# Optimization experiments

Measured on AMD Instinct MI355X. Metric: run time of the kernel, lower is better.

Reference implementation:

```python
import jax, jax.numpy as jnp
import numpy as np

HIDDEN = 1024
HEADS = 16
HEAD = HIDDEN // HEADS


def setup_inputs() -> dict:
    key = jax.random.key(0)
    ks = jax.random.split(key, 6)
    B, T = 2, 2048
    x = jax.random.normal(ks[0], (B, T, HIDDEN), dtype=jnp.float32)
    mask = jnp.ones((T, T), dtype=jnp.float32)
    s = 1.0 / np.sqrt(HIDDEN)
    Wqkv = jax.random.normal(ks[1], (HIDDEN, 3 * HIDDEN), dtype=jnp.float32) * s
    bqkv = jnp.zeros((3 * HIDDEN,), dtype=jnp.float32)
    Wproj = jax.random.normal(ks[2], (HIDDEN, HIDDEN), dtype=jnp.float32) * s
    bproj = jnp.zeros((HIDDEN,), dtype=jnp.float32)
    return {"x": x, "mask": mask, "Wqkv": Wqkv, "bqkv": bqkv,
            "Wproj": Wproj, "bproj": bproj}


def reference(x, mask, Wqkv, bqkv, Wproj, bproj):
    B, T, C = x.shape
    qkv = x @ Wqkv + bqkv                      # [B,T,3C]
    q, k, v = jnp.split(qkv, 3, axis=-1)
    def heads(t):                              # [B,T,C] -> [B,H,T,D]
        return t.reshape(B, T, HEADS, HEAD).transpose(0, 2, 1, 3)
    q, k, v = heads(q), heads(k), heads(v)
    scores = jnp.einsum('bhqd,bhkd->bhqk', q, k) / np.sqrt(HEAD)
    scores = jnp.where(mask == 0, -jnp.inf, scores)
    attn = jax.nn.softmax(scores, axis=-1)
    out = jnp.einsum('bhqk,bhkd->bhqd', attn, v)
    out = out.transpose(0, 2, 1, 3).reshape(B, T, C)
    return out @ Wproj + bproj
```

## Files before the change

kernel.cpp:

```cpp
#include <hip/hip_runtime.h>
#include <stdint.h>

#define HID 1024
#define NH 16
#define HD 64
#define BATCH 2
#define SEQ 2048
#define MR (BATCH*SEQ)
#define NQKV (3*HID)

typedef __attribute__((ext_vector_type(8))) _Float16 h16x8;
typedef __attribute__((ext_vector_type(2))) __fp16 fp16x2;
typedef __attribute__((ext_vector_type(8))) unsigned short u16x8;
typedef __attribute__((ext_vector_type(4))) float f32x4;

#if __has_builtin(__builtin_amdgcn_exp2f)
#define EXP2(x) __builtin_amdgcn_exp2f(x)
#else
#define EXP2(x) exp2f(x)
#endif

static __device__ __forceinline__ unsigned short f2h(float f) {
  union { _Float16 h; unsigned short u; } v; v.h = (_Float16)f; return v.u;
}
static __device__ __forceinline__ unsigned pk2(float a, float b) {
  union { fp16x2 h; unsigned u; } v;
  v.h = __builtin_amdgcn_cvt_pkrtz(a, b);
  return v.u;
}

typedef const __attribute__((address_space(1))) unsigned int glb_u32;
typedef __attribute__((address_space(3))) unsigned int lds_u32;
static __device__ __forceinline__ void cp16(const void* g, void* l) {
  __builtin_amdgcn_global_load_lds((glb_u32*)g, (lds_u32*)l, 16, 0, 0);
}

#define QSCL (0.125f * 1.44269504f)

__global__ __launch_bounds__(256) void k_cvt(const float4* __restrict__ src,
                                             ushort4* __restrict__ dst) {
  int i = blockIdx.x * 256 + threadIdx.x;
  float4 v = src[i];
  ushort4 h;
  h.x = f2h(v.x); h.y = f2h(v.y); h.z = f2h(v.z); h.w = f2h(v.w);
  dst[i] = h;
}

__global__ __launch_bounds__(256) void k_transpose_h(const float* __restrict__ src,
                                                     int R, int C,
                                                     unsigned short* __restrict__ dst) {
  __shared__ float tile[32][33];
  int tx = threadIdx.x, ty = threadIdx.y;
  int col0 = blockIdx.x * 32, row0 = blockIdx.y * 32;
  #pragma unroll
  for (int i = 0; i < 32; i += 8)
    tile[ty + i][tx] = src[(size_t)(row0 + ty + i) * C + col0 + tx];
  __syncthreads();
  #pragma unroll
  for (int i = 0; i < 32; i += 8) {
    float v = tile[tx][ty + i];
    dst[(size_t)(col0 + ty + i) * R + row0 + tx] = f2h(v);
  }
}

__global__ __launch_bounds__(256) void k_maskbits(const float* __restrict__ mask,
                                                  unsigned long long* __restrict__ mb) {
  int gw = blockIdx.x * 4 + (threadIdx.x >> 6);
  int lane = threadIdx.x & 63;
  float v = mask[(size_t)gw * 64 + lane];
  unsigned long long b = __ballot(v != 0.f);
  if (lane == 0) mb[gw] = b;
}

__global__ __launch_bounds__(256) void k_gemm_qkv(const unsigned short* __restrict__ A,
                                                  const unsigned short* __restrict__ Bt,
                                                  const float* __restrict__ bias,
                                                  unsigned short* __restrict__ Qp,
                                                  unsigned short* __restrict__ Kp,
                                                  unsigned short* __restrict__ Vt) {
  const int K = HID;
  int tid = threadIdx.x;
  int wave = tid >> 6, lane = tid & 63, quad = lane >> 4, l16 = lane & 15;
  int wm = wave >> 1, wn = wave & 1;
  int m0 = blockIdx.y * 128, n0 = blockIdx.x * 128;
  __shared__ __align__(16) unsigned short As[128 * 32], Bs[128 * 32];
  f32x4 acc[4][4] = {};
  for (int k0 = 0; k0 < K; k0 += 32) {
    __syncthreads();
    #pragma unroll
    for (int i = 0; i < 2; i++) {
      int c = tid + i * 256;
      int r = c >> 2, co = (c & 3) << 3;
      cp16(&A[(size_t)(m0 + r) * K + k0 + co], &As[c << 3]);
      cp16(&Bt[(size_t)(n0 + r) * K + k0 + co], &Bs[c << 3]);
    }
    __syncthreads();
    h16x8 af[4], bf[4];
    #pragma unroll
    for (int i = 0; i < 4; i++) {
      af[i] = *(const h16x8*)&As[(wm * 64 + i * 16 + l16) * 32 + quad * 8];
      bf[i] = *(const h16x8*)&Bs[(wn * 64 + i * 16 + l16) * 32 + quad * 8];
    }
    #pragma unroll
    for (int i = 0; i < 4; i++)
      #pragma unroll
      for (int j = 0; j < 4; j++)
        acc[i][j] = __builtin_amdgcn_mfma_f32_16x16x32_f16(af[i], bf[j], acc[i][j], 0, 0, 0);
  }
  #pragma unroll
  for (int j = 0; j < 4; j++) {
    int n = n0 + wn * 64 + j * 16 + l16;
    float bv = bias[n];
    int which = n >> 10;
    int rem = n & 1023;
    int h = rem >> 6, d = rem & 63;
    if (which == 2) {
      #pragma unroll
      for (int i = 0; i < 4; i++) {
        int m = m0 + wm * 64 + i * 16 + quad * 4;
        int b = m >> 11, t = m & 2047;
        uint2 tt;
        tt.x = pk2(acc[i][j][0] + bv, acc[i][j][1] + bv);
        tt.y = pk2(acc[i][j][2] + bv, acc[i][j][3] + bv);
        *(uint2*)&Vt[(size_t)(b * NH + h) * (SEQ * HD) + (size_t)d * SEQ + t] = tt;
      }
    } else {
      #pragma unroll
      for (int i = 0; i < 4; i++)
        #pragma unroll
        for (int r = 0; r < 4; r++) {
          int m = m0 + wm * 64 + i * 16 + quad * 4 + r;
          int b = m >> 11, t = m & 2047;
          float val = acc[i][j][r] + bv;
          int hb = b * NH + h;
          if (which == 0) Qp[(size_t)hb * (SEQ * HD) + (size_t)t * HD + d] = f2h(val * QSCL);
          else            Kp[(size_t)hb * (SEQ * HD) + (size_t)t * HD + d] = f2h(val);
        }
    }
  }
}

__global__ __launch_bounds__(256) void k_attn(const unsigned short* __restrict__ Qp,
                                              const unsigned short* __restrict__ Kp,
                                              const unsigned short* __restrict__ Vt,
                                              const unsigned long long* __restrict__ mb,
                                              unsigned short* __restrict__ AO) {
  int tid = threadIdx.x, wave = tid >> 6, lane = tid & 63, quad = lane >> 4, l16 = lane & 15;
  int bh = blockIdx.y, qbase = blockIdx.x * 64;
  const unsigned short* Qg = Qp + (size_t)bh * (SEQ * HD);
  const unsigned short* Kg = Kp + (size_t)bh * (SEQ * HD);
  const unsigned short* Vg = Vt + (size_t)bh * (SEQ * HD);
  __shared__ __align__(16) unsigned short smem[16896];
  unsigned short* Qs = smem;
  unsigned short* Ks = smem + 4096;
  unsigned short* Vs = smem + 8192;
  unsigned short* Ps = smem + 12288 + wave * (16 * 72);
  unsigned short* Os = smem + 4096;

  #pragma unroll
  for (int i = 0; i < 2; i++) {
    int c = tid + i * 256;
    int row = c >> 3, sc = ((c ^ row) & 7) << 3;
    cp16(&Qg[(size_t)(qbase + row) * HD + sc], &Qs[c << 3]);
  }
  int qrow = qbase + wave * 16 + l16;
  const unsigned long long* mrow = mb + (size_t)qrow * 32;
  float m_i = -3.0e38f, l_i = 0.f;
  f32x4 acc_o[4] = {};
  int x7 = l16 & 7;

  for (int kt = 0; kt < 32; kt++) {
    int kbase = kt * 64;
    __syncthreads();
    #pragma unroll
    for (int i = 0; i < 2; i++) {
      int c = tid + i * 256;
      int row = c >> 3, sc = ((c ^ row) & 7) << 3;
      cp16(&Kg[(size_t)(kbase + row) * HD + sc], &Ks[c << 3]);
      cp16(&Vg[(size_t)row * SEQ + kbase + sc], &Vs[c << 3]);
    }
    unsigned long long w = mrow[kt];
    __syncthreads();
    f32x4 s[4] = {};
    h16x8 bq[2];
    #pragma unroll
    for (int kk = 0; kk < 2; kk++)
      bq[kk] = *(const h16x8*)&Qs[(wave * 16 + l16) * 64 + (((kk * 4 + quad) ^ x7) << 3)];
    #pragma unroll
    for (int nt = 0; nt < 4; nt++)
      #pragma unroll
      for (int kk = 0; kk < 2; kk++) {
        h16x8 a = *(const h16x8*)&Ks[(nt * 16 + l16) * 64 + (((kk * 4 + quad) ^ x7) << 3)];
        s[nt] = __builtin_amdgcn_mfma_f32_16x16x32_f16(a, bq[kk], s[nt], 0, 0, 0);
      }
    if (!__all(w == ~0ULL)) {
      #pragma unroll
      for (int nt = 0; nt < 4; nt++)
        #pragma unroll
        for (int r = 0; r < 4; r++)
          if (!((w >> (nt * 16 + quad * 4 + r)) & 1ULL)) s[nt][r] = -1e30f;
    }
    float v = s[0][0];
    #pragma unroll
    for (int nt = 0; nt < 4; nt++)
      #pragma unroll
      for (int r = 0; r < 4; r++) v = fmaxf(v, s[nt][r]);
    v = fmaxf(v, __shfl_xor(v, 16));
    v = fmaxf(v, __shfl_xor(v, 32));
    float mnew = fmaxf(m_i, v);
    float alpha = EXP2(m_i - mnew);
    m_i = mnew;
    float lsum = 0.f;
    #pragma unroll
    for (int nt = 0; nt < 4; nt++)
      #pragma unroll
      for (int r = 0; r < 4; r++) {
        s[nt][r] = EXP2(s[nt][r] - mnew);
        lsum += s[nt][r];
      }
    lsum += __shfl_xor(lsum, 16);
    lsum += __shfl_xor(lsum, 32);
    l_i = l_i * alpha + lsum;
    #pragma unroll
    for (int nt = 0; nt < 4; nt++)
      #pragma unroll
      for (int r = 0; r < 4; r++) acc_o[nt][r] *= alpha;
    #pragma unroll
    for (int nt = 0; nt < 4; nt++) {
      uint2 t;
      t.x = pk2(s[nt][0], s[nt][1]);
      t.y = pk2(s[nt][2], s[nt][3]);
      *(uint2*)&Ps[l16 * 72 + nt * 16 + quad * 4] = t;
    }
    h16x8 bp[2];
    #pragma unroll
    for (int kk = 0; kk < 2; kk++)
      bp[kk] = *(const h16x8*)&Ps[l16 * 72 + kk * 32 + quad * 8];
    #pragma unroll
    for (int nt = 0; nt < 4; nt++)
      #pragma unroll
      for (int kk = 0; kk < 2; kk++) {
        h16x8 a = *(const h16x8*)&Vs[(nt * 16 + l16) * 64 + (((kk * 4 + quad) ^ x7) << 3)];
        acc_o[nt] = __builtin_amdgcn_mfma_f32_16x16x32_f16(a, bp[kk], acc_o[nt], 0, 0, 0);
      }
  }
  float rl = 1.0f / l_i;
  __syncthreads();
  #pragma unroll
  for (int nt = 0; nt < 4; nt++) {
    uint2 t;
    t.x = (unsigned)f2h(acc_o[nt][0] * rl) | ((unsigned)f2h(acc_o[nt][1] * rl) << 16);
    t.y = (unsigned)f2h(acc_o[nt][2] * rl) | ((unsigned)f2h(acc_o[nt][3] * rl) << 16);
    *(uint2*)&Os[(wave * 16 + l16) * 72 + nt * 16 + quad * 4] = t;
  }
  __syncthreads();
  int b = bh >> 4, h = bh & 15;
  #pragma unroll
  for (int i = 0; i < 2; i++) {
    int c = tid + i * 256;
    int row = c >> 3, co = (c & 7) << 3;
    u16x8 vv = *(const u16x8*)&Os[row * 72 + co];
    *(u16x8*)&AO[(size_t)(b * SEQ + qbase + row) * HID + h * HD + co] = vv;
  }
}

__global__ __launch_bounds__(256) void k_gemm_proj(const unsigned short* __restrict__ A,
                                                   const unsigned short* __restrict__ Bt,
                                                   const float* __restrict__ bias,
                                                   float* __restrict__ out) {
  const int K = HID;
  int tid = threadIdx.x;
  int wave = tid >> 6, lane = tid & 63, quad = lane >> 4, l16 = lane & 15;
  int wm = wave >> 1, wn = wave & 1;
  int m0 = blockIdx.y * 128, n0 = blockIdx.x * 128;
  __shared__ __align__(16) unsigned short As[128 * 32], Bs[128 * 32];
  f32x4 acc[4][4] = {};
  for (int k0 = 0; k0 < K; k0 += 32) {
    __syncthreads();
    #pragma unroll
    for (int i = 0; i < 2; i++) {
      int c = tid + i * 256;
      int r = c >> 2, co = (c & 3) << 3;
      cp16(&A[(size_t)(m0 + r) * K + k0 + co], &As[c << 3]);
      cp16(&Bt[(size_t)(n0 + r) * K + k0 + co], &Bs[c << 3]);
    }
    __syncthreads();
    h16x8 af[4], bf[4];
    #pragma unroll
    for (int i = 0; i < 4; i++) {
      af[i] = *(const h16x8*)&As[(wm * 64 + i * 16 + l16) * 32 + quad * 8];
      bf[i] = *(const h16x8*)&Bs[(wn * 64 + i * 16 + l16) * 32 + quad * 8];
    }
    #pragma unroll
    for (int i = 0; i < 4; i++)
      #pragma unroll
      for (int j = 0; j < 4; j++)
        acc[i][j] = __builtin_amdgcn_mfma_f32_16x16x32_f16(af[i], bf[j], acc[i][j], 0, 0, 0);
  }
  #pragma unroll
  for (int j = 0; j < 4; j++) {
    int n = n0 + wn * 64 + j * 16 + l16;
    float bv = bias[n];
    #pragma unroll
    for (int i = 0; i < 4; i++)
      #pragma unroll
      for (int r = 0; r < 4; r++) {
        int m = m0 + wm * 64 + i * 16 + quad * 4 + r;
        out[(size_t)m * HID + n] = acc[i][j][r] + bv;
      }
  }
}

extern "C" void kernel_launch(void* const* d_in, const int* in_sizes, int n_in,
                              void* d_out, int out_size, void* d_ws, size_t ws_size,
                              hipStream_t stream) {
  const float* x     = (const float*)d_in[0];
  const float* mask  = (const float*)d_in[1];
  const float* Wqkv  = (const float*)d_in[2];
  const float* bqkv  = (const float*)d_in[3];
  const float* Wproj = (const float*)d_in[4];
  const float* bproj = (const float*)d_in[5];
  float* out = (float*)d_out;

  uint8_t* ws = (uint8_t*)d_ws;
  size_t off = 0;
  auto alloc = [&](size_t bytes) -> void* {
    void* p = (void*)(ws + off);
    off += (bytes + 255) & ~(size_t)255;
    return p;
  };
  unsigned short* xh   = (unsigned short*)alloc((size_t)MR * HID * 2);
  unsigned short* WqT  = (unsigned short*)alloc((size_t)NQKV * HID * 2);
  unsigned short* WpT  = (unsigned short*)alloc((size_t)HID * HID * 2);
  unsigned short* Qp   = (unsigned short*)alloc((size_t)BATCH * NH * SEQ * HD * 2);
  unsigned short* Kp   = (unsigned short*)alloc((size_t)BATCH * NH * SEQ * HD * 2);
  unsigned short* Vtp  = (unsigned short*)alloc((size_t)BATCH * NH * SEQ * HD * 2);
  unsigned short* AO   = (unsigned short*)alloc((size_t)MR * HID * 2);
  unsigned long long* mb = (unsigned long long*)alloc((size_t)SEQ * (SEQ / 64) * 8);

  k_cvt<<<MR * HID / 4 / 256, 256, 0, stream>>>((const float4*)x, (ushort4*)xh);
  k_transpose_h<<<dim3(NQKV / 32, HID / 32), dim3(32, 8), 0, stream>>>(Wqkv, HID, NQKV, WqT);
  k_transpose_h<<<dim3(HID / 32, HID / 32), dim3(32, 8), 0, stream>>>(Wproj, HID, HID, WpT);
  k_maskbits<<<SEQ * (SEQ / 64) / 4, 256, 0, stream>>>(mask, mb);
  k_gemm_qkv<<<dim3(NQKV / 128, MR / 128), 256, 0, stream>>>(xh, WqT, bqkv, Qp, Kp, Vtp);
  k_attn<<<dim3(SEQ / 64, BATCH * NH), 256, 0, stream>>>(Qp, Kp, Vtp, mb, AO);
  k_gemm_proj<<<dim3(HID / 128, MR / 128), 256, 0, stream>>>(AO, WpT, bproj, out);
}
```

Baseline: 234.6 us.

## Double K-tile depth in GEMMs with XOR swizzle and process 128 keys per attention step

Both GEMM kernels now stage 64-wide K tiles instead of 32, with an XOR-swizzled shared-memory layout. This halves the number of barrier pairs per tile and is meant to reduce LDS bank conflicts on the fragment reads. The attention kernel loads two 64-key K/V tiles per iteration, which halves the barriers and online-softmax rescales, and it hoists the Q fragment loads out of the loop. In exchange it uses more shared memory, which may lower occupancy, and more registers for the doubled score fragments.

```diff
diff --git a/kernel.cpp b/kernel.cpp
--- a/kernel.cpp
+++ b/kernel.cpp
@@ -82,30 +82,34 @@
   int tid = threadIdx.x;
   int wave = tid >> 6, lane = tid & 63, quad = lane >> 4, l16 = lane & 15;
   int wm = wave >> 1, wn = wave & 1;
+  int x7 = l16 & 7;
   int m0 = blockIdx.y * 128, n0 = blockIdx.x * 128;
-  __shared__ __align__(16) unsigned short As[128 * 32], Bs[128 * 32];
+  __shared__ __align__(16) unsigned short As[128 * 64], Bs[128 * 64];
   f32x4 acc[4][4] = {};
-  for (int k0 = 0; k0 < K; k0 += 32) {
-    __syncthreads();
-    #pragma unroll
-    for (int i = 0; i < 2; i++) {
+  for (int k0 = 0; k0 < K; k0 += 64) {
+    __syncthreads();
+    #pragma unroll
+    for (int i = 0; i < 4; i++) {
       int c = tid + i * 256;
-      int r = c >> 2, co = (c & 3) << 3;
-      cp16(&A[(size_t)(m0 + r) * K + k0 + co], &As[c << 3]);
-      cp16(&Bt[(size_t)(n0 + r) * K + k0 + co], &Bs[c << 3]);
-    }
-    __syncthreads();
-    h16x8 af[4], bf[4];
-    #pragma unroll
-    for (int i = 0; i < 4; i++) {
-      af[i] = *(const h16x8*)&As[(wm * 64 + i * 16 + l16) * 32 + quad * 8];
-      bf[i] = *(const h16x8*)&Bs[(wn * 64 + i * 16 + l16) * 32 + quad * 8];
-    }
-    #pragma unroll
-    for (int i = 0; i < 4; i++)
-      #pragma unroll
-      for (int j = 0; j < 4; j++)
-        acc[i][j] = __builtin_amdgcn_mfma_f32_16x16x32_f16(af[i], bf[j], acc[i][j], 0, 0, 0);
+      int r = c >> 3, sc = ((c ^ r) & 7) << 3;
+      cp16(&A[(size_t)(m0 + r) * K + k0 + sc], &As[c << 3]);
+      cp16(&Bt[(size_t)(n0 + r) * K + k0 + sc], &Bs[c << 3]);
+    }
+    __syncthreads();
+    #pragma unroll
+    for (int kc = 0; kc < 2; kc++) {
+      h16x8 af[4], bf[4];
+      #pragma unroll
+      for (int i = 0; i < 4; i++) {
+        af[i] = *(const h16x8*)&As[(wm * 64 + i * 16 + l16) * 64 + (((kc * 4 + quad) ^ x7) << 3)];
+        bf[i] = *(const h16x8*)&Bs[(wn * 64 + i * 16 + l16) * 64 + (((kc * 4 + quad) ^ x7) << 3)];
+      }
+      #pragma unroll
+      for (int i = 0; i < 4; i++)
+        #pragma unroll
+        for (int j = 0; j < 4; j++)
+          acc[i][j] = __builtin_amdgcn_mfma_f32_16x16x32_f16(af[i], bf[j], acc[i][j], 0, 0, 0);
+    }
   }
   #pragma unroll
   for (int j = 0; j < 4; j++) {
@@ -150,12 +154,14 @@
   const unsigned short* Qg = Qp + (size_t)bh * (SEQ * HD);
   const unsigned short* Kg = Kp + (size_t)bh * (SEQ * HD);
   const unsigned short* Vg = Vt + (size_t)bh * (SEQ * HD);
-  __shared__ __align__(16) unsigned short smem[16896];
-  unsigned short* Qs = smem;
-  unsigned short* Ks = smem + 4096;
-  unsigned short* Vs = smem + 8192;
-  unsigned short* Ps = smem + 12288 + wave * (16 * 72);
-  unsigned short* Os = smem + 4096;
+  __shared__ __align__(16) unsigned short smem[25088];
+  unsigned short* Qs  = smem;
+  unsigned short* Ks0 = smem + 4096;
+  unsigned short* Ks1 = smem + 8192;
+  unsigned short* Vs0 = smem + 12288;
+  unsigned short* Vs1 = smem + 16384;
+  unsigned short* Ps  = smem + 20480 + wave * (16 * 72);
+  unsigned short* Os  = smem + 4096;
 
   #pragma unroll
   for (int i = 0; i < 2; i++) {
@@ -169,42 +175,50 @@
   f32x4 acc_o[4] = {};
   int x7 = l16 & 7;
 
-  for (int kt = 0; kt < 32; kt++) {
-    int kbase = kt * 64;
+  __syncthreads();
+  h16x8 bq[2];
+  #pragma unroll
+  for (int kk = 0; kk < 2; kk++)
+    bq[kk] = *(const h16x8*)&Qs[(wave * 16 + l16) * 64 + (((kk * 4 + quad) ^ x7) << 3)];
+
+  for (int kt = 0; kt < 16; kt++) {
+    int kbase = kt * 128;
     __syncthreads();
     #pragma unroll
     for (int i = 0; i < 2; i++) {
       int c = tid + i * 256;
       int row = c >> 3, sc = ((c ^ row) & 7) << 3;
-      cp16(&Kg[(size_t)(kbase + row) * HD + sc], &Ks[c << 3]);
-      cp16(&Vg[(size_t)row * SEQ + kbase + sc], &Vs[c << 3]);
-    }
-    unsigned long long w = mrow[kt];
-    __syncthreads();
-    f32x4 s[4] = {};
-    h16x8 bq[2];
-    #pragma unroll
-    for (int kk = 0; kk < 2; kk++)
-      bq[kk] = *(const h16x8*)&Qs[(wave * 16 + l16) * 64 + (((kk * 4 + quad) ^ x7) << 3)];
+      cp16(&Kg[(size_t)(kbase + row) * HD + sc],      &Ks0[c << 3]);
+      cp16(&Kg[(size_t)(kbase + 64 + row) * HD + sc], &Ks1[c << 3]);
+      cp16(&Vg[(size_t)row * SEQ + kbase + sc],       &Vs0[c << 3]);
+      cp16(&Vg[(size_t)row * SEQ + kbase + 64 + sc],  &Vs1[c << 3]);
+    }
+    unsigned long long w0 = mrow[2 * kt], w1 = mrow[2 * kt + 1];
+    __syncthreads();
+    f32x4 s0[4] = {}, s1[4] = {};
     #pragma unroll
     for (int nt = 0; nt < 4; nt++)
       #pragma unroll
       for (int kk = 0; kk < 2; kk++) {
-        h16x8 a = *(const h16x8*)&Ks[(nt * 16 + l16) * 64 + (((kk * 4 + quad) ^ x7) << 3)];
-        s[nt] = __builtin_amdgcn_mfma_f32_16x16x32_f16(a, bq[kk], s[nt], 0, 0, 0);
-      }
-    if (!__all(w == ~0ULL)) {
+        int fo = (nt * 16 + l16) * 64 + (((kk * 4 + quad) ^ x7) << 3);
+        s0[nt] = __builtin_amdgcn_mfma_f32_16x16x32_f16(*(const h16x8*)&Ks0[fo], bq[kk], s0[nt], 0, 0, 0);
+        s1[nt] = __builtin_amdgcn_mfma_f32_16x16x32_f16(*(const h16x8*)&Ks1[fo], bq[kk], s1[nt], 0, 0, 0);
+      }
+    if (!__all((w0 & w1) == ~0ULL)) {
       #pragma unroll
       for (int nt = 0; nt < 4; nt++)
         #pragma unroll
-        for (int r = 0; r < 4; r++)
-          if (!((w >> (nt * 16 + quad * 4 + r)) & 1ULL)) s[nt][r] = -1e30f;
-    }
-    float v = s[0][0];
+        for (int r = 0; r < 4; r++) {
+          int bit = nt * 16 + quad * 4 + r;
+          if (!((w0 >> bit) & 1ULL)) s0[nt][r] = -1e30f;
+          if (!((w1 >> bit) & 1ULL)) s1[nt][r] = -1e30f;
+        }
+    }
+    float v = s0[0][0];
     #pragma unroll
     for (int nt = 0; nt < 4; nt++)
       #pragma unroll
-      for (int r = 0; r < 4; r++) v = fmaxf(v, s[nt][r]);
+      for (int r = 0; r < 4; r++) { v = fmaxf(v, s0[nt][r]); v = fmaxf(v, s1[nt][r]); }
     v = fmaxf(v, __shfl_xor(v, 16));
     v = fmaxf(v, __shfl_xor(v, 32));
     float mnew = fmaxf(m_i, v);
@@ -215,8 +229,8 @@
     for (int nt = 0; nt < 4; nt++)
       #pragma unroll
       for (int r = 0; r < 4; r++) {
-        s[nt][r] = EXP2(s[nt][r] - mnew);
-        lsum += s[nt][r];
+        s0[nt][r] = EXP2(s0[nt][r] - mnew); lsum += s0[nt][r];
+        s1[nt][r] = EXP2(s1[nt][r] - mnew); lsum += s1[nt][r];
       }
     lsum += __shfl_xor(lsum, 16);
     lsum += __shfl_xor(lsum, 32);
@@ -228,21 +242,39 @@
     #pragma unroll
     for (int nt = 0; nt < 4; nt++) {
       uint2 t;
-      t.x = pk2(s[nt][0], s[nt][1]);
-      t.y = pk2(s[nt][2], s[nt][3]);
+      t.x = pk2(s0[nt][0], s0[nt][1]);
+      t.y = pk2(s0[nt][2], s0[nt][3]);
       *(uint2*)&Ps[l16 * 72 + nt * 16 + quad * 4] = t;
     }
-    h16x8 bp[2];
-    #pragma unroll
-    for (int kk = 0; kk < 2; kk++)
-      bp[kk] = *(const h16x8*)&Ps[l16 * 72 + kk * 32 + quad * 8];
-    #pragma unroll
-    for (int nt = 0; nt < 4; nt++)
-      #pragma unroll
-      for (int kk = 0; kk < 2; kk++) {
-        h16x8 a = *(const h16x8*)&Vs[(nt * 16 + l16) * 64 + (((kk * 4 + quad) ^ x7) << 3)];
-        acc_o[nt] = __builtin_amdgcn_mfma_f32_16x16x32_f16(a, bp[kk], acc_o[nt], 0, 0, 0);
-      }
+    {
+      h16x8 bp0 = *(const h16x8*)&Ps[l16 * 72 + quad * 8];
+      h16x8 bp1 = *(const h16x8*)&Ps[l16 * 72 + 32 + quad * 8];
+      #pragma unroll
+      for (int nt = 0; nt < 4; nt++) {
+        int fo0 = (nt * 16 + l16) * 64 + (((0 * 4 + quad) ^ x7) << 3);
+        int fo1 = (nt * 16 + l16) * 64 + (((1 * 4 + quad) ^ x7) << 3);
+        acc_o[nt] = __builtin_amdgcn_mfma_f32_16x16x32_f16(*(const h16x8*)&Vs0[fo0], bp0, acc_o[nt], 0, 0, 0);
+        acc_o[nt] = __builtin_amdgcn_mfma_f32_16x16x32_f16(*(const h16x8*)&Vs0[fo1], bp1, acc_o[nt], 0, 0, 0);
+      }
+    }
+    #pragma unroll
+    for (int nt = 0; nt < 4; nt++) {
+      uint2 t;
+      t.x = pk2(s1[nt][0], s1[nt][1]);
+      t.y = pk2(s1[nt][2], s1[nt][3]);
+      *(uint2*)&Ps[l16 * 72 + nt * 16 + quad * 4] = t;
+    }
+    {
+      h16x8 bp0 = *(const h16x8*)&Ps[l16 * 72 + quad * 8];
+      h16x8 bp1 = *(const h16x8*)&Ps[l16 * 72 + 32 + quad * 8];
+      #pragma unroll
+      for (int nt = 0; nt < 4; nt++) {
+        int fo0 = (nt * 16 + l16) * 64 + (((0 * 4 + quad) ^ x7) << 3);
+        int fo1 = (nt * 16 + l16) * 64 + (((1 * 4 + quad) ^ x7) << 3);
+        acc_o[nt] = __builtin_amdgcn_mfma_f32_16x16x32_f16(*(const h16x8*)&Vs1[fo0], bp0, acc_o[nt], 0, 0, 0);
+        acc_o[nt] = __builtin_amdgcn_mfma_f32_16x16x32_f16(*(const h16x8*)&Vs1[fo1], bp1, acc_o[nt], 0, 0, 0);
+      }
+    }
   }
   float rl = 1.0f / l_i;
   __syncthreads();
@@ -272,30 +304,34 @@
   int tid = threadIdx.x;
   int wave = tid >> 6, lane = tid & 63, quad = lane >> 4, l16 = lane & 15;
   int wm = wave >> 1, wn = wave & 1;
+  int x7 = l16 & 7;
   int m0 = blockIdx.y * 128, n0 = blockIdx.x * 128;
-  __shared__ __align__(16) unsigned short As[128 * 32], Bs[128 * 32];
+  __shared__ __align__(16) unsigned short As[128 * 64], Bs[128 * 64];
   f32x4 acc[4][4] = {};
-  for (int k0 = 0; k0 < K; k0 += 32) {
-    __syncthreads();
-    #pragma unroll
-    for (int i = 0; i < 2; i++) {
+  for (int k0 = 0; k0 < K; k0 += 64) {
+    __syncthreads();
+    #pragma unroll
+    for (int i = 0; i < 4; i++) {
       int c = tid + i * 256;
-      int r = c >> 2, co = (c & 3) << 3;
-      cp16(&A[(size_t)(m0 + r) * K + k0 + co], &As[c << 3]);
-      cp16(&Bt[(size_t)(n0 + r) * K + k0 + co], &Bs[c << 3]);
-    }
-    __syncthreads();
-    h16x8 af[4], bf[4];
-    #pragma unroll
-    for (int i = 0; i < 4; i++) {
-      af[i] = *(const h16x8*)&As[(wm * 64 + i * 16 + l16) * 32 + quad * 8];
-      bf[i] = *(const h16x8*)&Bs[(wn * 64 + i * 16 + l16) * 32 + quad * 8];
-    }
-    #pragma unroll
-    for (int i = 0; i < 4; i++)
-      #pragma unroll
-      for (int j = 0; j < 4; j++)
-        acc[i][j] = __builtin_amdgcn_mfma_f32_16x16x32_f16(af[i], bf[j], acc[i][j], 0, 0, 0);
+      int r = c >> 3, sc = ((c ^ r) & 7) << 3;
+      cp16(&A[(size_t)(m0 + r) * K + k0 + sc], &As[c << 3]);
+      cp16(&Bt[(size_t)(n0 + r) * K + k0 + sc], &Bs[c << 3]);
+    }
+    __syncthreads();
+    #pragma unroll
+    for (int kc = 0; kc < 2; kc++) {
+      h16x8 af[4], bf[4];
+      #pragma unroll
+      for (int i = 0; i < 4; i++) {
+        af[i] = *(const h16x8*)&As[(wm * 64 + i * 16 + l16) * 64 + (((kc * 4 + quad) ^ x7) << 3)];
+        bf[i] = *(const h16x8*)&Bs[(wn * 64 + i * 16 + l16) * 64 + (((kc * 4 + quad) ^ x7) << 3)];
+      }
+      #pragma unroll
+      for (int i = 0; i < 4; i++)
+        #pragma unroll
+        for (int j = 0; j < 4; j++)
+          acc[i][j] = __builtin_amdgcn_mfma_f32_16x16x32_f16(af[i], bf[j], acc[i][j], 0, 0, 0);
+    }
   }
   #pragma unroll
   for (int j = 0; j < 4; j++) {
```

Result: slower. 241.0 us (+2.8%).
